# Optimization experiments

Measured on AMD Instinct MI355X. Metric: run time of the kernel, lower is better.

## Reference

```python
import jax, jax.numpy as jnp
import numpy as np

EC = 32
N = 500000
DIV_EPS = 1e-8
NO_PENALTY_THRESH = 0.005

def _rotation_matrices(rpy):
    # rpy: [EC,3] roll-pitch-yaw -> [EC,3,3]
    c = jnp.cos(rpy); s = jnp.sin(rpy)
    cx, cy, cz = c[:, 0], c[:, 1], c[:, 2]
    sx, sy, sz = s[:, 0], s[:, 1], s[:, 2]
    R = jnp.stack([
        cz * cy, cz * sy * sx - sz * cx, cz * sy * cx + sz * sx,
        sz * cy, sz * sy * sx + cz * cx, sz * sy * cx - cz * sx,
        -sy,     cy * sx,                cy * cx,
    ], axis=-1)
    return R.reshape(rpy.shape[:-1] + (3, 3))

def _eval_rbf(samples, centers, radii, rotations):
    # samples [N,3], centers/radii/rotations [EC,3] -> [EC,N]
    d = 1.0 / (radii + DIV_EPS)                      # inverse diag covariances
    R = _rotation_matrices(rotations)                # [EC,3,3]
    inv_cov = jnp.einsum('eij,ej,ekj->eik', R, d, R) # R diag(d) R^T, symmetric
    diff = samples[None, :, :] - centers[:, None, :] # [EC,N,3]
    quad = jnp.einsum('eni,eij,enj->en', diff, inv_cov, diff)
    return jnp.exp(-0.5 * quad)

def setup_inputs() -> dict:
    key = jax.random.key(0)
    ks = jax.random.split(key, 7)
    u = lambda k, shape, lo, hi: jax.random.uniform(k, shape, jnp.float32, lo, hi)
    return {
        'world_space_points': jax.random.normal(ks[0], (N, 3), jnp.float32),
        'nerflet_activations': jax.random.normal(ks[1], (EC, N, 4), jnp.float32),
        'dists': jax.random.uniform(ks[2], (N, 1), jnp.float32),
        'constants': u(ks[3], (EC, 1), 10.0, 20.0),
        'centers': u(ks[4], (EC, 3), -0.45, 0.45),
        'radii': u(ks[5], (EC, 1), 0.05, 0.06),
        'rotations': u(ks[6], (EC, 3), -np.pi, np.pi),
    }

def reference(world_space_points, nerflet_activations, dists, constants, centers, radii, rotations):
    c = jnp.abs(constants)                            # [EC,1]
    r3 = jnp.tile(jnp.abs(radii), (1, 3))             # [EC,3]
    rbfs = _eval_rbf(world_space_points, centers, r3, rotations)[:, :, None]  # [EC,N,1]
    rbfs = rbfs * c[:, None, :]                       # scaled by |constants|
    penalty = jnp.mean(jnp.sum(jnp.abs(rbfs - NO_PENALTY_THRESH), axis=0))
    alpha = 1.0 - jnp.exp(-jax.nn.relu(nerflet_activations[..., -1:]) * dists[None])  # [EC,N,1]
    rgb = jax.nn.sigmoid(nerflet_activations[..., :3])
    na = jnp.concatenate([rgb, alpha], axis=-1)       # [EC,N,4]
    rbf_sums = jnp.sum(rbfs, axis=0, keepdims=True)   # [1,N,1]
    rbfs_norm = rbfs / (rbf_sums + 0.01)
    outputs = jnp.sum(na * rbfs_norm, axis=0)         # [N,4]
    return outputs, penalty
```

## Files before the change

### kernel.cpp

```cpp
#include <hip/hip_runtime.h>
#include <math.h>

#define EC 32
#define BLOCK 256


__global__ void ldif_setup_kernel(const float* __restrict__ constants,
                                  const float* __restrict__ centers,
                                  const float* __restrict__ radii,
                                  const float* __restrict__ rotations,
                                  float4* __restrict__ params) {
    int e = threadIdx.x;
    if (e >= EC) return;
    float r = fabsf(radii[e]);
    float dinv = 1.0f / (r + 1e-8f);
    float rx = rotations[3 * e + 0], ry = rotations[3 * e + 1], rz = rotations[3 * e + 2];
    float cx = cosf(rx), cy = cosf(ry), cz = cosf(rz);
    float sx = sinf(rx), sy = sinf(ry), sz = sinf(rz);
    float R00 = cz * cy, R01 = cz * sy * sx - sz * cx, R02 = cz * sy * cx + sz * sx;
    float R10 = sz * cy, R11 = sz * sy * sx + cz * cx, R12 = sz * sy * cx - cz * sx;
    float R20 = -sy,     R21 = cy * sx,                R22 = cy * cx;
    float ic00 = dinv * (R00 * R00 + R01 * R01 + R02 * R02);
    float ic11 = dinv * (R10 * R10 + R11 * R11 + R12 * R12);
    float ic22 = dinv * (R20 * R20 + R21 * R21 + R22 * R22);
    float ic01 = dinv * (R00 * R10 + R01 * R11 + R02 * R12);
    float ic02 = dinv * (R00 * R20 + R01 * R21 + R02 * R22);
    float ic12 = dinv * (R10 * R20 + R11 * R21 + R12 * R22);
    const float NH = -0.72134752044f;
    float Axx = NH * ic00, Ayy = NH * ic11, Azz = NH * ic22;
    float Axy = 2.0f * NH * ic01, Axz = 2.0f * NH * ic02, Ayz = 2.0f * NH * ic12;
    float lc = log2f(fabsf(constants[e]));
    params[3 * e + 0] = make_float4(centers[3 * e + 0], centers[3 * e + 1], centers[3 * e + 2], lc);
    params[3 * e + 1] = make_float4(Axx, Ayy, Azz, Axy);
    params[3 * e + 2] = make_float4(Axz, Ayz, 0.0f, 0.0f);
}

__global__ __launch_bounds__(BLOCK) void ldif_main_kernel(
    const float* __restrict__ pts,
    const float4* __restrict__ act,
    const float* __restrict__ dists,
    const float4* __restrict__ params,
    float4* __restrict__ out,
    float* __restrict__ partials,
    int n) {
    __shared__ float4 sp[EC * 3];
    __shared__ float red[BLOCK];
    int tid = threadIdx.x;
    if (tid < EC * 3) sp[tid] = params[tid];
    __syncthreads();

    long long i = (long long)blockIdx.x * BLOCK + tid;
    float pen = 0.0f;
    if (i < n) {
        float px = pts[3 * i + 0];
        float py = pts[3 * i + 1];
        float pz = pts[3 * i + 2];
        float dl = dists[i] * 1.44269504f;

        float rbf[EC];
        float s = 0.0f;
#pragma unroll
        for (int e = 0; e < EC; ++e) {
            float4 p0 = sp[3 * e + 0];
            float4 p1 = sp[3 * e + 1];
            float4 p2 = sp[3 * e + 2];
            float dx = px - p0.x, dy = py - p0.y, dz = pz - p0.z;
            float q = (p1.x * dx + p1.w * dy + p2.x * dz) * dx
                    + (p1.y * dy + p2.y * dz) * dy
                    + (p1.z * dz) * dz
                    + p0.w;
            float v = __builtin_amdgcn_exp2f(q);
            rbf[e] = v;
            s += v;
            pen += fabsf(v - 0.005f);
        }
        float rn = __builtin_amdgcn_rcpf(s + 0.01f);

        float a0 = 0.0f, a1 = 0.0f, a2 = 0.0f, a3 = 0.0f;
#pragma unroll 8
        for (int e = 0; e < EC; ++e) {
            float4 a = act[(size_t)e * (size_t)n + (size_t)i];
            float w = rbf[e] * rn;
            float s0 = __builtin_amdgcn_rcpf(1.0f + __builtin_amdgcn_exp2f(-1.44269504f * a.x));
            float s1 = __builtin_amdgcn_rcpf(1.0f + __builtin_amdgcn_exp2f(-1.44269504f * a.y));
            float s2 = __builtin_amdgcn_rcpf(1.0f + __builtin_amdgcn_exp2f(-1.44269504f * a.z));
            float al = 1.0f - __builtin_amdgcn_exp2f(-fmaxf(a.w, 0.0f) * dl);
            a0 += w * s0;
            a1 += w * s1;
            a2 += w * s2;
            a3 += w * al;
        }
        out[i] = make_float4(a0, a1, a2, a3);
    }

    red[tid] = pen;
    __syncthreads();
    for (int st = BLOCK / 2; st > 0; st >>= 1) {
        if (tid < st) red[tid] += red[tid + st];
        __syncthreads();
    }
    if (tid == 0) partials[blockIdx.x] = red[0];
}

__global__ __launch_bounds__(BLOCK) void ldif_reduce_kernel(
    const float* __restrict__ partials, int nparts, float* __restrict__ out, int n) {
    __shared__ double rd[BLOCK];
    int tid = threadIdx.x;
    double s = 0.0;
    for (int j = tid; j < nparts; j += BLOCK) s += (double)partials[j];
    rd[tid] = s;
    __syncthreads();
    for (int st = BLOCK / 2; st > 0; st >>= 1) {
        if (tid < st) rd[tid] += rd[tid + st];
        __syncthreads();
    }
    if (tid == 0) out[0] = (float)(rd[0] / (double)n);
}

extern "C" void kernel_launch(void* const* d_in, const int* in_sizes, int n_in,
                              void* d_out, int out_size, void* d_ws, size_t ws_size,
                              hipStream_t stream) {
    const float* pts       = (const float*)d_in[0];
    const float* act       = (const float*)d_in[1];
    const float* dists     = (const float*)d_in[2];
    const float* constants = (const float*)d_in[3];
    const float* centers   = (const float*)d_in[4];
    const float* radii     = (const float*)d_in[5];
    const float* rotations = (const float*)d_in[6];
    float* out = (float*)d_out;

    int n = in_sizes[0] / 3;
    float4* params  = (float4*)d_ws;
    float* partials = (float*)((char*)d_ws + 2048);

    int nblocks = (n + BLOCK - 1) / BLOCK;

    ldif_setup_kernel<<<1, 64, 0, stream>>>(constants, centers, radii, rotations, params);
    ldif_main_kernel<<<nblocks, BLOCK, 0, stream>>>(
        pts, (const float4*)act, dists, params, (float4*)out, partials, n);
    ldif_reduce_kernel<<<1, BLOCK, 0, stream>>>(partials, nblocks, out + (size_t)4 * n, n);
}
```

Measured before the change: 58.67 us.

## Fuse parameter setup into main kernel and merge RBF and blend loops

Drops the separate setup kernel: each block's first 32 threads compute the inverse-covariance parameters directly into shared memory. The RBF evaluation and the activation blending now share one loop, with normalization applied once at the end, so the per-point rbf[32] register array goes away. Activation loads and output stores use nontemporal builtins. This saves one launch and register pressure, at the cost of redundant trig work in every block and some reordering of the floating-point sums.

```diff
diff --git a/kernel.cpp b/kernel.cpp
--- a/kernel.cpp
+++ b/kernel.cpp
@@ -4,49 +4,44 @@
 #define EC 32
 #define BLOCK 256
 
-
-__global__ void ldif_setup_kernel(const float* __restrict__ constants,
-                                  const float* __restrict__ centers,
-                                  const float* __restrict__ radii,
-                                  const float* __restrict__ rotations,
-                                  float4* __restrict__ params) {
-    int e = threadIdx.x;
-    if (e >= EC) return;
-    float r = fabsf(radii[e]);
-    float dinv = 1.0f / (r + 1e-8f);
-    float rx = rotations[3 * e + 0], ry = rotations[3 * e + 1], rz = rotations[3 * e + 2];
-    float cx = cosf(rx), cy = cosf(ry), cz = cosf(rz);
-    float sx = sinf(rx), sy = sinf(ry), sz = sinf(rz);
-    float R00 = cz * cy, R01 = cz * sy * sx - sz * cx, R02 = cz * sy * cx + sz * sx;
-    float R10 = sz * cy, R11 = sz * sy * sx + cz * cx, R12 = sz * sy * cx - cz * sx;
-    float R20 = -sy,     R21 = cy * sx,                R22 = cy * cx;
-    float ic00 = dinv * (R00 * R00 + R01 * R01 + R02 * R02);
-    float ic11 = dinv * (R10 * R10 + R11 * R11 + R12 * R12);
-    float ic22 = dinv * (R20 * R20 + R21 * R21 + R22 * R22);
-    float ic01 = dinv * (R00 * R10 + R01 * R11 + R02 * R12);
-    float ic02 = dinv * (R00 * R20 + R01 * R21 + R02 * R22);
-    float ic12 = dinv * (R10 * R20 + R11 * R21 + R12 * R22);
-    const float NH = -0.72134752044f;
-    float Axx = NH * ic00, Ayy = NH * ic11, Azz = NH * ic22;
-    float Axy = 2.0f * NH * ic01, Axz = 2.0f * NH * ic02, Ayz = 2.0f * NH * ic12;
-    float lc = log2f(fabsf(constants[e]));
-    params[3 * e + 0] = make_float4(centers[3 * e + 0], centers[3 * e + 1], centers[3 * e + 2], lc);
-    params[3 * e + 1] = make_float4(Axx, Ayy, Azz, Axy);
-    params[3 * e + 2] = make_float4(Axz, Ayz, 0.0f, 0.0f);
-}
+typedef float fvec4 __attribute__((ext_vector_type(4)));
 
 __global__ __launch_bounds__(BLOCK) void ldif_main_kernel(
     const float* __restrict__ pts,
-    const float4* __restrict__ act,
+    const fvec4* __restrict__ act,
     const float* __restrict__ dists,
-    const float4* __restrict__ params,
-    float4* __restrict__ out,
+    const float* __restrict__ constants,
+    const float* __restrict__ centers,
+    const float* __restrict__ radii,
+    const float* __restrict__ rotations,
+    fvec4* __restrict__ out,
     float* __restrict__ partials,
     int n) {
     __shared__ float4 sp[EC * 3];
     __shared__ float red[BLOCK];
     int tid = threadIdx.x;
-    if (tid < EC * 3) sp[tid] = params[tid];
+    if (tid < EC) {
+        int e = tid;
+        float r = fabsf(radii[e]);
+        float dinv = 1.0f / (r + 1e-8f);
+        float rx = rotations[3 * e + 0], ry = rotations[3 * e + 1], rz = rotations[3 * e + 2];
+        float cx = cosf(rx), cy = cosf(ry), cz = cosf(rz);
+        float sx = sinf(rx), sy = sinf(ry), sz = sinf(rz);
+        float R00 = cz * cy, R01 = cz * sy * sx - sz * cx, R02 = cz * sy * cx + sz * sx;
+        float R10 = sz * cy, R11 = sz * sy * sx + cz * cx, R12 = sz * sy * cx - cz * sx;
+        float R20 = -sy,     R21 = cy * sx,                R22 = cy * cx;
+        float ic00 = dinv * (R00 * R00 + R01 * R01 + R02 * R02);
+        float ic11 = dinv * (R10 * R10 + R11 * R11 + R12 * R12);
+        float ic22 = dinv * (R20 * R20 + R21 * R21 + R22 * R22);
+        float ic01 = dinv * (R00 * R10 + R01 * R11 + R02 * R12);
+        float ic02 = dinv * (R00 * R20 + R01 * R21 + R02 * R22);
+        float ic12 = dinv * (R10 * R20 + R11 * R21 + R12 * R22);
+        const float NH = -0.72134752044f;
+        float lc = log2f(fabsf(constants[e]));
+        sp[3 * e + 0] = make_float4(centers[3 * e + 0], centers[3 * e + 1], centers[3 * e + 2], lc);
+        sp[3 * e + 1] = make_float4(NH * ic00, NH * ic11, NH * ic22, 2.0f * NH * ic01);
+        sp[3 * e + 2] = make_float4(2.0f * NH * ic02, 2.0f * NH * ic12, 0.0f, 0.0f);
+    }
     __syncthreads();
 
     long long i = (long long)blockIdx.x * BLOCK + tid;
@@ -57,10 +52,11 @@
         float pz = pts[3 * i + 2];
         float dl = dists[i] * 1.44269504f;
 
-        float rbf[EC];
         float s = 0.0f;
-#pragma unroll
+        float a0 = 0.0f, a1 = 0.0f, a2 = 0.0f, a3 = 0.0f;
+#pragma unroll 8
         for (int e = 0; e < EC; ++e) {
+            fvec4 a = __builtin_nontemporal_load(&act[(size_t)e * (size_t)n + (size_t)i]);
             float4 p0 = sp[3 * e + 0];
             float4 p1 = sp[3 * e + 1];
             float4 p2 = sp[3 * e + 2];
@@ -70,27 +66,21 @@
                     + (p1.z * dz) * dz
                     + p0.w;
             float v = __builtin_amdgcn_exp2f(q);
-            rbf[e] = v;
             s += v;
             pen += fabsf(v - 0.005f);
-        }
-        float rn = __builtin_amdgcn_rcpf(s + 0.01f);
-
-        float a0 = 0.0f, a1 = 0.0f, a2 = 0.0f, a3 = 0.0f;
-#pragma unroll 8
-        for (int e = 0; e < EC; ++e) {
-            float4 a = act[(size_t)e * (size_t)n + (size_t)i];
-            float w = rbf[e] * rn;
             float s0 = __builtin_amdgcn_rcpf(1.0f + __builtin_amdgcn_exp2f(-1.44269504f * a.x));
             float s1 = __builtin_amdgcn_rcpf(1.0f + __builtin_amdgcn_exp2f(-1.44269504f * a.y));
             float s2 = __builtin_amdgcn_rcpf(1.0f + __builtin_amdgcn_exp2f(-1.44269504f * a.z));
             float al = 1.0f - __builtin_amdgcn_exp2f(-fmaxf(a.w, 0.0f) * dl);
-            a0 += w * s0;
-            a1 += w * s1;
-            a2 += w * s2;
-            a3 += w * al;
+            a0 += v * s0;
+            a1 += v * s1;
+            a2 += v * s2;
+            a3 += v * al;
         }
-        out[i] = make_float4(a0, a1, a2, a3);
+        float rn = __builtin_amdgcn_rcpf(s + 0.01f);
+        fvec4 o;
+        o.x = a0 * rn; o.y = a1 * rn; o.z = a2 * rn; o.w = a3 * rn;
+        __builtin_nontemporal_store(o, &out[i]);
     }
 
     red[tid] = pen;
@@ -130,13 +120,12 @@
     float* out = (float*)d_out;
 
     int n = in_sizes[0] / 3;
-    float4* params  = (float4*)d_ws;
-    float* partials = (float*)((char*)d_ws + 2048);
+    float* partials = (float*)d_ws;
 
     int nblocks = (n + BLOCK - 1) / BLOCK;
 
-    ldif_setup_kernel<<<1, 64, 0, stream>>>(constants, centers, radii, rotations, params);
     ldif_main_kernel<<<nblocks, BLOCK, 0, stream>>>(
-        pts, (const float4*)act, dists, params, (float4*)out, partials, n);
+        pts, (const fvec4*)act, dists, constants, centers, radii, rotations,
+        (fvec4*)out, partials, n);
     ldif_reduce_kernel<<<1, BLOCK, 0, stream>>>(partials, nblocks, out + (size_t)4 * n, n);
 }
```

Result: faster. 51.13 us (-12.9%).
